# Optimization experiments

Hardware: AMD Instinct MI355X
Metric: run time of the kernel (lower is better)

## Reference

```python
import jax, jax.numpy as jnp
import numpy as np


def setup_inputs() -> dict:
    key = jax.random.key(0)
    k1, k2, k3, k4 = jax.random.split(key, 4)
    B, T, D, L = 32, 30, 512, 196
    x = jax.random.normal(k1, (B, T, D), dtype=jnp.float32)
    wordemb = jax.random.normal(k2, (B, T, D), dtype=jnp.float32)
    imgsfeats = jax.random.normal(k3, (B, L, D), dtype=jnp.float32)
    v_w = jax.random.normal(k4, (D,), dtype=jnp.float32) * (1.0 / np.sqrt(D))
    v_b = jnp.zeros((1,), dtype=jnp.float32)
    return {"x": x, "wordemb": wordemb, "imgsfeats": imgsfeats, "v_w": v_w, "v_b": v_b}


def reference(x, wordemb, imgsfeats, v_w, v_b):
    # x, wordemb: (B, T=30, D=512); imgsfeats: (B, L, D)
    # y = imgsfeats.transpose(2,1) broadcast over T: (B, 1, D, L)
    y = jnp.transpose(imgsfeats, (0, 2, 1))[:, None, :, :]          # (B,1,D,L)
    att = jnp.tanh(x[:, :, :, None] + y + wordemb[:, :, :, None])   # (B,T,D,L)
    # score: linear D->1 applied along D
    e = jnp.einsum('btdl,d->btl', att, v_w) + v_b[0]                 # (B,T,L)
    alpha = jax.nn.softmax(e, axis=-1)                               # (B,T,L)
    # context = sum_l y * alpha -> (B,T,D)
    context = jnp.einsum('bld,btl->btd', imgsfeats, alpha)
    return context
```

## Files before the change

### kernel.cpp

```cpp
#include <hip/hip_runtime.h>

namespace {
constexpr int kB = 32, kT = 30, kD = 512, kL = 196;
constexpr float kK = 2.8853900817779268f;
constexpr size_t kGsz = (size_t)kB * kT * kL;

#define PAIR(ex, ey, fx, fy, vx, vy, acc)                                   \
  {                                                                         \
    const float u_ = fmaf(ex, fx, 1.f);                                     \
    const float v_ = fmaf(ey, fy, 1.f);                                     \
    acc = fmaf(fmaf(v_, vx, u_ * vy), __builtin_amdgcn_rcpf(u_ * v_), acc); \
  }

__global__ __launch_bounds__(512) void k_score(const float* __restrict__ x,
                                               const float* __restrict__ w,
                                               const float* __restrict__ img,
                                               const float* __restrict__ vw,
                                               float* __restrict__ g8) {
  __shared__ __align__(16) float4 Fl4[16 * 64];
  __shared__ __align__(16) float4 El4[32 * 16];
  __shared__ __align__(16) float4 vwl4[16];
  __shared__ __align__(16) float sc[4 * 8 * 64];
  int n = blockIdx.x;
  const int bg = n & 7;
  int m = n >> 3;
  const int bi = m & 3; m >>= 2;
  const int lc = m % 3;
  const int dqg = m / 3;
  const int b = bg * 4 + bi;
  const int l0 = lc * 64, d0 = dqg * 64;
  const int tid = threadIdx.x;
#pragma unroll
  for (int k = 0; k < 2; ++k) {
    const int i = tid + k * 512;
    const int l = i >> 4, c = i & 15;
    const float4 v =
        *(const float4*)(img + ((size_t)(b * kL + l0 + l)) * kD + d0 + 4 * c);
    float4 o;
    o.x = __builtin_amdgcn_exp2f(kK * v.x);
    o.y = __builtin_amdgcn_exp2f(kK * v.y);
    o.z = __builtin_amdgcn_exp2f(kK * v.z);
    o.w = __builtin_amdgcn_exp2f(kK * v.w);
    Fl4[c * 64 + (l ^ (c & 7))] = o;
  }
  {
    const int row = tid >> 4, c4 = tid & 15;
    const int tc = (row < kT) ? row : kT - 1;
    const size_t gi = ((size_t)(b * kT + tc)) * kD + d0 + 4 * c4;
    const float4 xv = *(const float4*)(x + gi);
    const float4 wv4 = *(const float4*)(w + gi);
    float4 e;
    e.x = __builtin_amdgcn_exp2f(kK * (xv.x + wv4.x));
    e.y = __builtin_amdgcn_exp2f(kK * (xv.y + wv4.y));
    e.z = __builtin_amdgcn_exp2f(kK * (xv.z + wv4.z));
    e.w = __builtin_amdgcn_exp2f(kK * (xv.w + wv4.w));
    El4[row * 16 + c4] = e;
  }
  if (tid < 16) vwl4[tid] = *(const float4*)(vw + d0 + 4 * tid);
  __syncthreads();
  const int lane = tid & 63, wva = tid >> 6;
  const int tg = wva & 3, dh = wva >> 2;
  const int r0 = tg * 8;
  const float4* Ew = &El4[r0 * 16];
  float acc[8];
#pragma unroll
  for (int tt = 0; tt < 8; ++tt) acc[tt] = 0.f;
#pragma unroll
  for (int s = 0; s < 8; ++s) {
    const int c4 = dh * 8 + s;
    const float4 f = Fl4[c4 * 64 + (lane ^ s)];
    const float4 vv = vwl4[c4];
#pragma unroll
    for (int tt = 0; tt < 8; ++tt) {
      const float4 E = Ew[tt * 16 + c4];
      PAIR(E.x, E.y, f.x, f.y, vv.x, vv.y, acc[tt]);
      PAIR(E.z, E.w, f.z, f.w, vv.z, vv.w, acc[tt]);
    }
  }
  if (dh == 1) {
#pragma unroll
    for (int tt = 0; tt < 8; ++tt) sc[(tg * 8 + tt) * 64 + lane] = acc[tt];
  }
  __syncthreads();
  if (dh == 0) {
    float* gp =
        g8 + (size_t)dqg * kGsz + ((size_t)(b * kT + r0)) * kL + l0 + lane;
#pragma unroll
    for (int tt = 0; tt < 8; ++tt) {
      if (r0 + tt < kT) {
        gp[(size_t)tt * kL] = acc[tt] + sc[(tg * 8 + tt) * 64 + lane];
      }
    }
  }
}

__global__ __launch_bounds__(256) void k_ctxa(const float* __restrict__ g8,
                                              const float* __restrict__ x,
                                              const float* __restrict__ w,
                                              const float* __restrict__ img,
                                              const float* __restrict__ vw,
                                              float* __restrict__ out) {
  __shared__ float AL2[5][200];
  __shared__ __align__(16) float red[4][5][256];
  int n = blockIdx.x;
  const int bg = n & 7;
  int m = n >> 3;
  const int bi = m & 3; m >>= 2;
  const int tg = m % 6;
  const int dh = m / 6;
  const int b = bg * 4 + bi;
  const int t0 = tg * 5, d0 = dh * 256;
  const int tid = threadIdx.x;
  const int lane = tid & 63;
  const int wv = tid >> 6;
#pragma unroll 1
  for (int r = wv; r < 5; r += 4) {
    const int t = t0 + r;
    const int l4 = lane & 3, dc = lane >> 2;
    const float* ir = img + ((size_t)(b * kL + 192 + l4)) * kD + dc * 32;
    const float* xr = x + ((size_t)(b * kT + t)) * kD + dc * 32;
    const float* wr = w + ((size_t)(b * kT + t)) * kD + dc * 32;
    const float* vr = vw + dc * 32;
    float tgv = 0.f;
#pragma unroll
    for (int k = 0; k < 8; ++k) {
      const float4 iv = *(const float4*)(ir + 4 * k);
      const float4 xv = *(const float4*)(xr + 4 * k);
      const float4 wv4 = *(const float4*)(wr + 4 * k);
      const float4 vv = *(const float4*)(vr + 4 * k);
      const float fx = __builtin_amdgcn_exp2f(kK * iv.x);
      const float fy = __builtin_amdgcn_exp2f(kK * iv.y);
      const float fz = __builtin_amdgcn_exp2f(kK * iv.z);
      const float fw = __builtin_amdgcn_exp2f(kK * iv.w);
      const float ex = __builtin_amdgcn_exp2f(kK * (xv.x + wv4.x));
      const float ey = __builtin_amdgcn_exp2f(kK * (xv.y + wv4.y));
      const float ez = __builtin_amdgcn_exp2f(kK * (xv.z + wv4.z));
      const float ew = __builtin_amdgcn_exp2f(kK * (xv.w + wv4.w));
      PAIR(ex, ey, fx, fy, vv.x, vv.y, tgv);
      PAIR(ez, ew, fz, fw, vv.z, vv.w, tgv);
    }
#pragma unroll
    for (int mm = 4; mm < 64; mm <<= 1) tgv += __shfl_xor(tgv, mm, 64);
    const size_t base = ((size_t)(b * kT + t)) * kL;
    float q0 = 0.f, q1 = 0.f, q2 = 0.f;
#pragma unroll
    for (int p = 0; p < 8; ++p) {
      const float* gp = g8 + (size_t)p * kGsz + base;
      q0 += gp[lane];
      q1 += gp[lane + 64];
      q2 += gp[lane + 128];
    }
    q0 *= kK; q1 *= kK; q2 *= kK;
    float q3 = (lane < 4) ? tgv * kK : __builtin_inff();
    float mn = fminf(fminf(q0, q1), fminf(q2, q3));
#pragma unroll
    for (int mm = 1; mm < 64; mm <<= 1) mn = fminf(mn, __shfl_xor(mn, mm, 64));
    const float e0 = __builtin_amdgcn_exp2f(mn - q0);
    const float e1 = __builtin_amdgcn_exp2f(mn - q1);
    const float e2 = __builtin_amdgcn_exp2f(mn - q2);
    const float e3 = (lane < 4) ? __builtin_amdgcn_exp2f(mn - q3) : 0.f;
    float s = e0 + e1 + e2 + e3;
#pragma unroll
    for (int mm = 1; mm < 64; mm <<= 1) s += __shfl_xor(s, mm, 64);
    const float rs = __builtin_amdgcn_rcpf(s);
    AL2[r][lane] = e0 * rs;
    AL2[r][lane + 64] = e1 * rs;
    AL2[r][lane + 128] = e2 * rs;
    if (lane < 4) AL2[r][lane + 192] = e3 * rs;
  }
  __syncthreads();
  const int lru = __builtin_amdgcn_readfirstlane(wv);
  const float* ip = img + ((size_t)(b * kL + lru * 49)) * kD + d0 + 4 * lane;
  const int lb = lru * 49;
  float4 acc[5];
#pragma unroll
  for (int j = 0; j < 5; ++j) acc[j] = {0.f, 0.f, 0.f, 0.f};
  auto loadI = [&](float4* dst, int bb) {
#pragma unroll
    for (int j = 0; j < 4; ++j)
      dst[j] = *(const float4*)(ip + (size_t)(bb * 4 + j) * kD);
  };
  auto compI = [&](const float4* f, int bb) {
#pragma unroll
    for (int j = 0; j < 4; ++j) {
      const int l = lb + bb * 4 + j;
      const float a0 = AL2[0][l];
      const float a1 = AL2[1][l];
      const float a2 = AL2[2][l];
      const float a3 = AL2[3][l];
      const float a4 = AL2[4][l];
      acc[0].x = fmaf(f[j].x, a0, acc[0].x); acc[0].y = fmaf(f[j].y, a0, acc[0].y);
      acc[0].z = fmaf(f[j].z, a0, acc[0].z); acc[0].w = fmaf(f[j].w, a0, acc[0].w);
      acc[1].x = fmaf(f[j].x, a1, acc[1].x); acc[1].y = fmaf(f[j].y, a1, acc[1].y);
      acc[1].z = fmaf(f[j].z, a1, acc[1].z); acc[1].w = fmaf(f[j].w, a1, acc[1].w);
      acc[2].x = fmaf(f[j].x, a2, acc[2].x); acc[2].y = fmaf(f[j].y, a2, acc[2].y);
      acc[2].z = fmaf(f[j].z, a2, acc[2].z); acc[2].w = fmaf(f[j].w, a2, acc[2].w);
      acc[3].x = fmaf(f[j].x, a3, acc[3].x); acc[3].y = fmaf(f[j].y, a3, acc[3].y);
      acc[3].z = fmaf(f[j].z, a3, acc[3].z); acc[3].w = fmaf(f[j].w, a3, acc[3].w);
      acc[4].x = fmaf(f[j].x, a4, acc[4].x); acc[4].y = fmaf(f[j].y, a4, acc[4].y);
      acc[4].z = fmaf(f[j].z, a4, acc[4].z); acc[4].w = fmaf(f[j].w, a4, acc[4].w);
    }
  };
  float4 fA[4], fB[4];
  loadI(fA, 0);
#pragma unroll
  for (int bb = 0; bb < 12; ++bb) {
    if (bb + 1 < 12) {
      if ((bb + 1) & 1) loadI(fB, bb + 1);
      else loadI(fA, bb + 1);
    }
    if (bb & 1) compI(fB, bb);
    else compI(fA, bb);
  }
  {
    const float4 v = *(const float4*)(ip + (size_t)48 * kD);
    const int l = lb + 48;
    const float a0 = AL2[0][l], a1 = AL2[1][l], a2 = AL2[2][l],
                a3 = AL2[3][l], a4 = AL2[4][l];
    acc[0].x = fmaf(v.x, a0, acc[0].x); acc[0].y = fmaf(v.y, a0, acc[0].y);
    acc[0].z = fmaf(v.z, a0, acc[0].z); acc[0].w = fmaf(v.w, a0, acc[0].w);
    acc[1].x = fmaf(v.x, a1, acc[1].x); acc[1].y = fmaf(v.y, a1, acc[1].y);
    acc[1].z = fmaf(v.z, a1, acc[1].z); acc[1].w = fmaf(v.w, a1, acc[1].w);
    acc[2].x = fmaf(v.x, a2, acc[2].x); acc[2].y = fmaf(v.y, a2, acc[2].y);
    acc[2].z = fmaf(v.z, a2, acc[2].z); acc[2].w = fmaf(v.w, a2, acc[2].w);
    acc[3].x = fmaf(v.x, a3, acc[3].x); acc[3].y = fmaf(v.y, a3, acc[3].y);
    acc[3].z = fmaf(v.z, a3, acc[3].z); acc[3].w = fmaf(v.w, a3, acc[3].w);
    acc[4].x = fmaf(v.x, a4, acc[4].x); acc[4].y = fmaf(v.y, a4, acc[4].y);
    acc[4].z = fmaf(v.z, a4, acc[4].z); acc[4].w = fmaf(v.w, a4, acc[4].w);
  }
#pragma unroll
  for (int j = 0; j < 5; ++j) *(float4*)&red[wv][j][4 * lane] = acc[j];
  __syncthreads();
#pragma unroll
  for (int j = 0; j < 5; ++j) {
    const float s =
        red[0][j][tid] + red[1][j][tid] + red[2][j][tid] + red[3][j][tid];
    out[((size_t)(b * kT + t0 + j)) * kD + d0 + tid] = s;
  }
}
}

extern "C" void kernel_launch(void* const* d_in, const int* in_sizes, int n_in,
                              void* d_out, int out_size, void* d_ws, size_t ws_size,
                              hipStream_t stream) {
  const float* x = (const float*)d_in[0];
  const float* wordemb = (const float*)d_in[1];
  const float* img = (const float*)d_in[2];
  const float* vw = (const float*)d_in[3];
  float* out = (float*)d_out;
  float* g8 = (float*)d_ws;
  hipLaunchKernelGGL(k_score, dim3(768), dim3(512), 0, stream, x, wordemb, img,
                     vw, g8);
  hipLaunchKernelGGL(k_ctxa, dim3(384), dim3(256), 0, stream, g8, x, wordemb,
                     img, vw, out);
}
```

Baseline: 28.71 us.

## Retile score kernel to full L per block and widen context blocks

```diff
diff --git a/kernel.cpp b/kernel.cpp
--- a/kernel.cpp
+++ b/kernel.cpp
@@ -4,6 +4,7 @@
 constexpr int kB = 32, kT = 30, kD = 512, kL = 196;
 constexpr float kK = 2.8853900817779268f;
 constexpr size_t kGsz = (size_t)kB * kT * kL;
+constexpr int kNP = 16;
 
 #define PAIR(ex, ey, fx, fy, vx, vy, acc)                                   \
   {                                                                         \
@@ -16,35 +17,34 @@
                                                const float* __restrict__ w,
                                                const float* __restrict__ img,
                                                const float* __restrict__ vw,
-                                               float* __restrict__ g8) {
-  __shared__ __align__(16) float4 Fl4[16 * 64];
-  __shared__ __align__(16) float4 El4[32 * 16];
-  __shared__ __align__(16) float4 vwl4[16];
-  __shared__ __align__(16) float sc[4 * 8 * 64];
+                                               float* __restrict__ g16) {
+  __shared__ __align__(16) float4 Fl4[8 * 192];
+  __shared__ __align__(16) float4 El4[32 * 8];
+  __shared__ __align__(16) float4 vwl4[8];
+  __shared__ float sc[4 * 8 * 192];
   int n = blockIdx.x;
   const int bg = n & 7;
-  int m = n >> 3;
-  const int bi = m & 3; m >>= 2;
-  const int lc = m % 3;
-  const int dqg = m / 3;
+  const int m = n >> 3;
+  const int bi = m & 3;
+  const int dqs = m >> 2;
   const int b = bg * 4 + bi;
-  const int l0 = lc * 64, d0 = dqg * 64;
+  const int d0 = dqs * 32;
   const int tid = threadIdx.x;
 #pragma unroll
-  for (int k = 0; k < 2; ++k) {
+  for (int k = 0; k < 3; ++k) {
     const int i = tid + k * 512;
-    const int l = i >> 4, c = i & 15;
+    const int l = i >> 3, c4 = i & 7;
     const float4 v =
-        *(const float4*)(img + ((size_t)(b * kL + l0 + l)) * kD + d0 + 4 * c);
+        *(const float4*)(img + ((size_t)(b * kL + l)) * kD + d0 + 4 * c4);
     float4 o;
     o.x = __builtin_amdgcn_exp2f(kK * v.x);
     o.y = __builtin_amdgcn_exp2f(kK * v.y);
     o.z = __builtin_amdgcn_exp2f(kK * v.z);
     o.w = __builtin_amdgcn_exp2f(kK * v.w);
-    Fl4[c * 64 + (l ^ (c & 7))] = o;
-  }
-  {
-    const int row = tid >> 4, c4 = tid & 15;
+    Fl4[c4 * 192 + ((l & ~7) | ((l ^ c4) & 7))] = o;
+  }
+  if (tid < 256) {
+    const int row = tid >> 3, c4 = tid & 7;
     const int tc = (row < kT) ? row : kT - 1;
     const size_t gi = ((size_t)(b * kT + tc)) * kD + d0 + 4 * c4;
     const float4 xv = *(const float4*)(x + gi);
@@ -54,68 +54,80 @@
     e.y = __builtin_amdgcn_exp2f(kK * (xv.y + wv4.y));
     e.z = __builtin_amdgcn_exp2f(kK * (xv.z + wv4.z));
     e.w = __builtin_amdgcn_exp2f(kK * (xv.w + wv4.w));
-    El4[row * 16 + c4] = e;
-  }
-  if (tid < 16) vwl4[tid] = *(const float4*)(vw + d0 + 4 * tid);
+    El4[row * 8 + c4] = e;
+  }
+  if (tid < 8) vwl4[tid] = *(const float4*)(vw + d0 + 4 * tid);
   __syncthreads();
   const int lane = tid & 63, wva = tid >> 6;
   const int tg = wva & 3, dh = wva >> 2;
   const int r0 = tg * 8;
-  const float4* Ew = &El4[r0 * 16];
-  float acc[8];
-#pragma unroll
-  for (int tt = 0; tt < 8; ++tt) acc[tt] = 0.f;
-#pragma unroll
-  for (int s = 0; s < 8; ++s) {
-    const int c4 = dh * 8 + s;
-    const float4 f = Fl4[c4 * 64 + (lane ^ s)];
+  float acc[8][3];
+#pragma unroll
+  for (int tt = 0; tt < 8; ++tt)
+#pragma unroll
+    for (int j = 0; j < 3; ++j) acc[tt][j] = 0.f;
+#pragma unroll
+  for (int s = 0; s < 4; ++s) {
+    const int c4 = dh * 4 + s;
     const float4 vv = vwl4[c4];
+    const int sw = (lane ^ c4) & 7;
+    const int bse = (lane & 56) + sw;
+    float4 f[3];
+#pragma unroll
+    for (int j = 0; j < 3; ++j) f[j] = Fl4[c4 * 192 + bse + 64 * j];
 #pragma unroll
     for (int tt = 0; tt < 8; ++tt) {
-      const float4 E = Ew[tt * 16 + c4];
-      PAIR(E.x, E.y, f.x, f.y, vv.x, vv.y, acc[tt]);
-      PAIR(E.z, E.w, f.z, f.w, vv.z, vv.w, acc[tt]);
+      const float4 E = El4[(r0 + tt) * 8 + c4];
+#pragma unroll
+      for (int j = 0; j < 3; ++j) {
+        PAIR(E.x, E.y, f[j].x, f[j].y, vv.x, vv.y, acc[tt][j]);
+        PAIR(E.z, E.w, f[j].z, f[j].w, vv.z, vv.w, acc[tt][j]);
+      }
     }
   }
   if (dh == 1) {
 #pragma unroll
-    for (int tt = 0; tt < 8; ++tt) sc[(tg * 8 + tt) * 64 + lane] = acc[tt];
+    for (int tt = 0; tt < 8; ++tt)
+#pragma unroll
+      for (int j = 0; j < 3; ++j)
+        sc[(r0 + tt) * 192 + lane + 64 * j] = acc[tt][j];
   }
   __syncthreads();
   if (dh == 0) {
-    float* gp =
-        g8 + (size_t)dqg * kGsz + ((size_t)(b * kT + r0)) * kL + l0 + lane;
+    float* gp = g16 + (size_t)dqs * kGsz + ((size_t)(b * kT + r0)) * kL + lane;
 #pragma unroll
     for (int tt = 0; tt < 8; ++tt) {
       if (r0 + tt < kT) {
-        gp[(size_t)tt * kL] = acc[tt] + sc[(tg * 8 + tt) * 64 + lane];
+#pragma unroll
+        for (int j = 0; j < 3; ++j) {
+          gp[(size_t)tt * kL + 64 * j] =
+              acc[tt][j] + sc[(r0 + tt) * 192 + lane + 64 * j];
+        }
       }
     }
   }
 }
 
-__global__ __launch_bounds__(256) void k_ctxa(const float* __restrict__ g8,
+__global__ __launch_bounds__(512) void k_ctxa(const float* __restrict__ g16,
                                               const float* __restrict__ x,
                                               const float* __restrict__ w,
                                               const float* __restrict__ img,
                                               const float* __restrict__ vw,
                                               float* __restrict__ out) {
   __shared__ float AL2[5][200];
-  __shared__ __align__(16) float red[4][5][256];
+  __shared__ __align__(16) float red[8][5][256];
   int n = blockIdx.x;
   const int bg = n & 7;
-  int m = n >> 3;
-  const int bi = m & 3; m >>= 2;
-  const int tg = m % 6;
-  const int dh = m / 6;
+  const int m = n >> 3;
+  const int bi = m & 3;
+  const int tgc = m >> 2;
   const int b = bg * 4 + bi;
-  const int t0 = tg * 5, d0 = dh * 256;
+  const int t0 = tgc * 5;
   const int tid = threadIdx.x;
   const int lane = tid & 63;
   const int wv = tid >> 6;
-#pragma unroll 1
-  for (int r = wv; r < 5; r += 4) {
-    const int t = t0 + r;
+  if (wv < 5) {
+    const int t = t0 + wv;
     const int l4 = lane & 3, dc = lane >> 2;
     const float* ir = img + ((size_t)(b * kL + 192 + l4)) * kD + dc * 32;
     const float* xr = x + ((size_t)(b * kT + t)) * kD + dc * 32;
@@ -144,8 +156,8 @@
     const size_t base = ((size_t)(b * kT + t)) * kL;
     float q0 = 0.f, q1 = 0.f, q2 = 0.f;
 #pragma unroll
-    for (int p = 0; p < 8; ++p) {
-      const float* gp = g8 + (size_t)p * kGsz + base;
+    for (int p = 0; p < kNP; ++p) {
+      const float* gp = g16 + (size_t)p * kGsz + base;
       q0 += gp[lane];
       q1 += gp[lane + 64];
       q2 += gp[lane + 128];
@@ -163,15 +175,17 @@
 #pragma unroll
     for (int mm = 1; mm < 64; mm <<= 1) s += __shfl_xor(s, mm, 64);
     const float rs = __builtin_amdgcn_rcpf(s);
-    AL2[r][lane] = e0 * rs;
-    AL2[r][lane + 64] = e1 * rs;
-    AL2[r][lane + 128] = e2 * rs;
-    if (lane < 4) AL2[r][lane + 192] = e3 * rs;
-  }
-  __syncthreads();
-  const int lru = __builtin_amdgcn_readfirstlane(wv);
-  const float* ip = img + ((size_t)(b * kL + lru * 49)) * kD + d0 + 4 * lane;
-  const int lb = lru * 49;
+    AL2[wv][lane] = e0 * rs;
+    AL2[wv][lane + 64] = e1 * rs;
+    AL2[wv][lane + 128] = e2 * rs;
+    if (lane < 4) AL2[wv][lane + 192] = e3 * rs;
+  }
+  __syncthreads();
+  const int lq = __builtin_amdgcn_readfirstlane(wv & 3);
+  const int dh = __builtin_amdgcn_readfirstlane(wv >> 2);
+  const int d0 = dh * 256;
+  const int lb = lq * 49;
+  const float* ip = img + ((size_t)(b * kL + lb)) * kD + d0 + 4 * lane;
   float4 acc[5];
 #pragma unroll
   for (int j = 0; j < 5; ++j) acc[j] = {0.f, 0.f, 0.f, 0.f};
@@ -231,11 +245,12 @@
 #pragma unroll
   for (int j = 0; j < 5; ++j) *(float4*)&red[wv][j][4 * lane] = acc[j];
   __syncthreads();
+  const int col = tid & 255, dhh = tid >> 8;
 #pragma unroll
   for (int j = 0; j < 5; ++j) {
-    const float s =
-        red[0][j][tid] + red[1][j][tid] + red[2][j][tid] + red[3][j][tid];
-    out[((size_t)(b * kT + t0 + j)) * kD + d0 + tid] = s;
+    const float s = red[dhh * 4 + 0][j][col] + red[dhh * 4 + 1][j][col] +
+                    red[dhh * 4 + 2][j][col] + red[dhh * 4 + 3][j][col];
+    out[((size_t)(b * kT + t0 + j)) * kD + dhh * 256 + col] = s;
   }
 }
 }
@@ -248,9 +263,9 @@
   const float* img = (const float*)d_in[2];
   const float* vw = (const float*)d_in[3];
   float* out = (float*)d_out;
-  float* g8 = (float*)d_ws;
-  hipLaunchKernelGGL(k_score, dim3(768), dim3(512), 0, stream, x, wordemb, img,
-                     vw, g8);
-  hipLaunchKernelGGL(k_ctxa, dim3(384), dim3(256), 0, stream, g8, x, wordemb,
+  float* g16 = (float*)d_ws;
+  hipLaunchKernelGGL(k_score, dim3(512), dim3(512), 0, stream, x, wordemb, img,
+                     vw, g16);
+  hipLaunchKernelGGL(k_ctxa, dim3(192), dim3(512), 0, stream, g16, x, wordemb,
                      img, vw, out);
 }
```

New measurement: 28.86 us. Within noise of the previous version (+0.5%).
